# Kernel optimization log

Measured on AMD Instinct MI355X. Metric: run time of the kernel, lower is better.

The kernel has to match this reference:

```python
import jax, jax.numpy as jnp
import numpy as np

B, T, D = 4, 2048, 1024
H = 16
HD = D // H  # 64

def setup_inputs() -> dict:
    key = jax.random.key(0)
    k1, k2, k3 = jax.random.split(key, 3)
    x = jax.random.normal(k1, (B, T, D), dtype=jnp.float32)
    # torch nn.Linear weight layout: [out_features, in_features]
    w_qkv = jax.random.normal(k2, (3 * D, D), dtype=jnp.float32) * (D ** -0.5)
    w_proj = jax.random.normal(k3, (D, D), dtype=jnp.float32) * (D ** -0.5)
    return {"x": x, "w_qkv": w_qkv, "w_proj": w_proj}

def reference(x, w_qkv, w_proj):
    b, t, c = x.shape
    qkv = jnp.einsum('btc,oc->bto', x, w_qkv)  # [b,t,3c]
    q, k, v = jnp.split(qkv, 3, axis=-1)
    # [b,h,t,hd]
    q = q.reshape(b, t, H, HD).transpose(0, 2, 1, 3)
    k = k.reshape(b, t, H, HD).transpose(0, 2, 1, 3)
    v = v.reshape(b, t, H, HD).transpose(0, 2, 1, 3)
    att = jnp.einsum('bhqd,bhkd->bhqk', q, k) / (HD ** 0.5)
    causal = jnp.tril(jnp.ones((t, t), dtype=bool))
    att = jnp.where(causal, att, -jnp.inf)
    att = jax.nn.softmax(att, axis=-1)
    y = jnp.einsum('bhqk,bhkd->bhqd', att, v)
    y = y.transpose(0, 2, 1, 3).reshape(b, t, c)
    return jnp.einsum('btc,oc->bto', y, w_proj)
```

## Files before the change

kernel.cpp:

```cpp
#include <hip/hip_runtime.h>
#include <cstdint>
#include <cstddef>


typedef __bf16 bf16;
typedef __bf16 bf16x4 __attribute__((ext_vector_type(4)));
typedef __bf16 bf16x8 __attribute__((ext_vector_type(8)));
typedef float  f32x4  __attribute__((ext_vector_type(4)));
typedef float  fvec4  __attribute__((ext_vector_type(4)));
typedef unsigned u32x2 __attribute__((ext_vector_type(2)));

typedef __attribute__((address_space(1))) const void global_cv;
typedef __attribute__((address_space(3))) void lds_v;

#define MFMA16(a, b, c) __builtin_amdgcn_mfma_f32_16x16x32_bf16((a), (b), (c), 0, 0, 0)

#define QSCALE 0.18033688f

__device__ __forceinline__ void async_ld16(const bf16* g, bf16* l) {
  __builtin_amdgcn_global_load_lds((global_cv*)g, (lds_v*)l, 16, 0, 0);
}

__device__ __forceinline__ int swz_off(int row, int col) {
  int sr = (row & 7) ^ ((row >> 3) & 7);
  return row * 64 + ((((col >> 3) ^ sr) & 7) * 8) + (col & 7);
}

__device__ __forceinline__ unsigned cvt_pk(float lo, float hi) {
  unsigned r;
  asm("v_cvt_pk_bf16_f32 %0, %1, %2" : "=v"(r) : "v"(lo), "v"(hi));
  return r;
}

__device__ __forceinline__ bf16x8 cvt8(const float* p) {
  fvec4 u = *(const fvec4*)p;
  fvec4 v = *(const fvec4*)(p + 4);
  bf16x8 r;
  r[0] = (bf16)u[0]; r[1] = (bf16)u[1]; r[2] = (bf16)u[2]; r[3] = (bf16)u[3];
  r[4] = (bf16)v[0]; r[5] = (bf16)v[1]; r[6] = (bf16)v[2]; r[7] = (bf16)v[3];
  return r;
}

__global__ void cvt_f32_bf16(const float* __restrict__ s, bf16* __restrict__ d,
                             int n8) {
  int i = blockIdx.x * 256 + threadIdx.x;
  if (i < n8) *(bf16x8*)(d + (size_t)i * 8) = cvt8(s + (size_t)i * 8);
}

__device__ __forceinline__ void qkv_scatter(const f32x4 acc[4][4], int m0, int n0,
                                            int wm, int wn, int quad, int l15,
                                            bf16* Qo, bf16* Ko, bf16* Vo) {
  const int which = n0 >> 10;
  if (which == 2) {
#pragma unroll
    for (int i = 0; i < 4; ++i) {
      const int m = m0 + wm + i * 16 + quad * 4;
      const int b = m >> 11;
      const int t = m & 2047;
#pragma unroll
      for (int j = 0; j < 4; ++j) {
        const int n1 = (n0 + wn + j * 16 + l15) & 1023;
        const int h  = n1 >> 6;
        const int d  = n1 & 63;
        bf16x4 v;
#pragma unroll
        for (int r = 0; r < 4; ++r) v[r] = (bf16)acc[i][j][r];
        *(bf16x4*)(Vo + ((size_t)(b * 16 + h) * 64 + d) * 2048 + t) = v;
      }
    }
    return;
  }
  bf16* dst = (which == 0) ? Qo : Ko;
  const float scale = (which == 0) ? QSCALE : 1.0f;
#pragma unroll
  for (int i = 0; i < 4; ++i) {
    const int m = m0 + wm + i * 16 + quad * 4;
#pragma unroll
    for (int j = 0; j < 4; ++j) {
      const int n  = n0 + wn + j * 16 + l15;
      const int n1 = n & 1023;
      const int h  = n1 >> 6;
      const int d  = n1 & 63;
#pragma unroll
      for (int r = 0; r < 4; ++r) {
        const int mm = m + r;
        const int b  = mm >> 11;
        const int t  = mm & 2047;
        dst[(((size_t)(b * 16 + h)) * 2048 + t) * 64 + d] =
            (bf16)(acc[i][j][r] * scale);
      }
    }
  }
}

__global__ __launch_bounds__(256, 2)
void gemm_qkv_a(const bf16* __restrict__ A, const bf16* __restrict__ B,
                bf16* __restrict__ Qo, bf16* __restrict__ Ko,
                bf16* __restrict__ Vo) {
  __shared__ __align__(16) bf16 As[128 * 32];
  __shared__ __align__(16) bf16 Bs[128 * 32];
  const int K = 1024;

  const int tid  = threadIdx.x;
  const int lane = tid & 63;
  const int wave = tid >> 6;
  const int quad = lane >> 4;
  const int l15  = lane & 15;
  const int wm   = (wave >> 1) * 64;
  const int wn   = (wave & 1) * 64;
  const int m0   = blockIdx.y * 128;
  const int n0   = blockIdx.x * 128;

  f32x4 acc[4][4];
#pragma unroll
  for (int i = 0; i < 4; ++i)
#pragma unroll
    for (int j = 0; j < 4; ++j) acc[i][j] = f32x4{0.f, 0.f, 0.f, 0.f};

  const int r0 = tid >> 2;
  const int c0 = (tid & 3) * 8;
  const bf16* ag0 = A + (size_t)(m0 + r0) * K + c0;
  const bf16* ag1 = A + (size_t)(m0 + 64 + r0) * K + c0;
  const bf16* bg0 = B + (size_t)(n0 + r0) * K + c0;
  const bf16* bg1 = B + (size_t)(n0 + 64 + r0) * K + c0;
  const int lo0 = (wave * 64) * 8;
  const int lo1 = (256 + wave * 64) * 8;

  for (int k0 = 0; k0 < K; k0 += 32) {
    __syncthreads();
    async_ld16(ag0 + k0, As + lo0);
    async_ld16(ag1 + k0, As + lo1);
    async_ld16(bg0 + k0, Bs + lo0);
    async_ld16(bg1 + k0, Bs + lo1);
    __syncthreads();

    bf16x8 af[4], bfr[4];
#pragma unroll
    for (int i = 0; i < 4; ++i)
      af[i] = *(const bf16x8*)(As + (wm + i * 16 + l15) * 32 + quad * 8);
#pragma unroll
    for (int j = 0; j < 4; ++j)
      bfr[j] = *(const bf16x8*)(Bs + (wn + j * 16 + l15) * 32 + quad * 8);
#pragma unroll
    for (int i = 0; i < 4; ++i)
#pragma unroll
      for (int j = 0; j < 4; ++j)
        acc[i][j] = MFMA16(af[i], bfr[j], acc[i][j]);
  }
  qkv_scatter(acc, m0, n0, wm, wn, quad, l15, Qo, Ko, Vo);
}

__global__ __launch_bounds__(256, 2)
void gemm_qkv_f(const float* __restrict__ A, const float* __restrict__ B,
                bf16* __restrict__ Qo, bf16* __restrict__ Ko,
                bf16* __restrict__ Vo) {
  __shared__ __align__(16) bf16 As[128 * 32];
  __shared__ __align__(16) bf16 Bs[128 * 32];
  const int K = 1024;

  const int tid  = threadIdx.x;
  const int lane = tid & 63;
  const int wave = tid >> 6;
  const int quad = lane >> 4;
  const int l15  = lane & 15;
  const int wm   = (wave >> 1) * 64;
  const int wn   = (wave & 1) * 64;
  const int m0   = blockIdx.y * 128;
  const int n0   = blockIdx.x * 128;

  f32x4 acc[4][4];
#pragma unroll
  for (int i = 0; i < 4; ++i)
#pragma unroll
    for (int j = 0; j < 4; ++j) acc[i][j] = f32x4{0.f, 0.f, 0.f, 0.f};

  const int r0 = tid >> 2;
  const int c0 = (tid & 3) * 8;
  const size_t aoff0 = (size_t)(m0 + r0) * K + c0;
  const size_t aoff1 = (size_t)(m0 + 64 + r0) * K + c0;
  const size_t boff0 = (size_t)(n0 + r0) * K + c0;
  const size_t boff1 = (size_t)(n0 + 64 + r0) * K + c0;

  for (int k0 = 0; k0 < K; k0 += 32) {
    bf16x8 va0 = cvt8(A + aoff0 + k0);
    bf16x8 va1 = cvt8(A + aoff1 + k0);
    bf16x8 vb0 = cvt8(B + boff0 + k0);
    bf16x8 vb1 = cvt8(B + boff1 + k0);
    __syncthreads();
    *(bf16x8*)(As + tid * 8)        = va0;
    *(bf16x8*)(As + 2048 + tid * 8) = va1;
    *(bf16x8*)(Bs + tid * 8)        = vb0;
    *(bf16x8*)(Bs + 2048 + tid * 8) = vb1;
    __syncthreads();

    bf16x8 af[4], bfr[4];
#pragma unroll
    for (int i = 0; i < 4; ++i)
      af[i] = *(const bf16x8*)(As + (wm + i * 16 + l15) * 32 + quad * 8);
#pragma unroll
    for (int j = 0; j < 4; ++j)
      bfr[j] = *(const bf16x8*)(Bs + (wn + j * 16 + l15) * 32 + quad * 8);
#pragma unroll
    for (int i = 0; i < 4; ++i)
#pragma unroll
      for (int j = 0; j < 4; ++j)
        acc[i][j] = MFMA16(af[i], bfr[j], acc[i][j]);
  }
  qkv_scatter(acc, m0, n0, wm, wn, quad, l15, Qo, Ko, Vo);
}

__global__ __launch_bounds__(256, 4)
void attn(const bf16* __restrict__ Q, const bf16* __restrict__ Kk,
          const bf16* __restrict__ Vt, bf16* __restrict__ Y) {
  __shared__ __align__(16) bf16 Ks[2][64 * 64];
  __shared__ __align__(16) bf16 Vs[2][64 * 64];
  __shared__ __align__(16) bf16 Ps[4 * 16 * 64];

  const int tid  = threadIdx.x;
  const int wave = tid >> 6;
  const int lane = tid & 63;
  const int quad = lane >> 4;
  const int l15  = lane & 15;

  const int lin  = (int)blockIdx.x + ((int)blockIdx.y << 4);
  const int slot = lin >> 3;
  const int bh   = (lin & 7) * 8 + (slot >> 4);
  const int p    = slot & 15;
  const int b    = bh >> 4;
  const int h    = bh & 15;

  const bf16* Qb = Q  + (size_t)bh * (2048 * 64);
  const bf16* Kb = Kk + (size_t)bh * (2048 * 64);
  const bf16* Vb = Vt + (size_t)bh * (2048 * 64);
  char* Pw = (char*)(Ps + wave * (16 * 64));

  const int r0s = wave * 8 + (lane >> 3);
  const int r1s = r0s + 32;
  const int qch = lane & 7;
  const int co0 = (((qch ^ ((r0s & 7) ^ ((r0s >> 3) & 7)))) & 7) * 8;
  const int co1 = (((qch ^ ((r1s & 7) ^ ((r1s >> 3) & 7)))) & 7) * 8;
  const bf16* kg0 = Kb + (size_t)r0s * 64 + co0;
  const bf16* kg1 = Kb + (size_t)r1s * 64 + co1;
  const bf16* vg0 = Vb + (size_t)r0s * 2048 + co0;
  const bf16* vg1 = Vb + (size_t)r1s * 2048 + co1;
  const int ldsw = wave * 512;

  const int psx   = l15 & 7;
  const int prowb = l15 * 128;
  const int pr0   = prowb + ((quad ^ psx) << 4);
  const int pr1   = prowb + (((4 + quad) ^ psx) << 4);

  const float NEG = -1e30f;

#pragma unroll 1
  for (int pass = 0; pass < 2; ++pass) {
    const int qt = pass ? (31 - p) : p;
    const int q0 = qt * 64;

    const bf16* qp = Qb + (size_t)(q0 + wave * 16 + l15) * 64 + quad * 8;
    bf16x8 qa0 = *(const bf16x8*)qp;
    bf16x8 qa1 = *(const bf16x8*)(qp + 32);

    f32x4 l4 = {0.f, 0.f, 0.f, 0.f};
    f32x4 o[4];
#pragma unroll
    for (int j = 0; j < 4; ++j) o[j] = f32x4{0.f, 0.f, 0.f, 0.f};

    async_ld16(kg0, Ks[0] + ldsw);
    async_ld16(kg1, Ks[0] + 2048 + ldsw);
    async_ld16(vg0, Vs[0] + ldsw);
    async_ld16(vg1, Vs[0] + 2048 + ldsw);
    __syncthreads();

#pragma unroll 1
    for (int kt = 0; kt <= qt; ++kt) {
      const int cur = kt & 1;
      const int k0  = kt * 64;

      if (kt < qt) {
        const int kn = k0 + 64;
        async_ld16(kg0 + (size_t)kn * 64, Ks[cur ^ 1] + ldsw);
        async_ld16(kg1 + (size_t)kn * 64, Ks[cur ^ 1] + 2048 + ldsw);
        async_ld16(vg0 + kn, Vs[cur ^ 1] + ldsw);
        async_ld16(vg1 + kn, Vs[cur ^ 1] + 2048 + ldsw);
      }

      f32x4 s[4];
      __builtin_amdgcn_s_setprio(1);
#pragma unroll
      for (int j = 0; j < 4; ++j) {
        const int kvr = j * 16 + l15;
        bf16x8 k0f = *(const bf16x8*)(Ks[cur] + swz_off(kvr, quad * 8));
        bf16x8 k1f = *(const bf16x8*)(Ks[cur] + swz_off(kvr, 32 + quad * 8));
        f32x4 z = {0.f, 0.f, 0.f, 0.f};
        z = MFMA16(k0f, qa0, z);
        z = MFMA16(k1f, qa1, z);
        s[j] = z;
      }
      __builtin_amdgcn_s_setprio(0);

      if (kt == qt) {
        const int qloc = wave * 16 + l15;
#pragma unroll
        for (int j = 0; j < 4; ++j) {
#pragma unroll
          for (int r = 0; r < 4; ++r) {
            if (16 * j + 4 * quad + r > qloc) s[j][r] = NEG;
          }
        }
      }

#pragma unroll
      for (int j = 0; j < 4; ++j) {
#pragma unroll
        for (int r = 0; r < 4; ++r) s[j][r] = exp2f(s[j][r]);
        l4 += s[j];
      }

#pragma unroll
      for (int j = 0; j < 4; ++j) {
        u32x2 pk;
        pk[0] = cvt_pk(s[j][0], s[j][1]);
        pk[1] = cvt_pk(s[j][2], s[j][3]);
        const int C = 2 * j + (quad >> 1);
        *(u32x2*)(Pw + prowb + (((C ^ psx) << 4) | ((quad & 1) << 3))) = pk;
      }

      bf16x8 pf0 = *(const bf16x8*)(Pw + pr0);
      bf16x8 pf1 = *(const bf16x8*)(Pw + pr1);

      __builtin_amdgcn_s_setprio(1);
#pragma unroll
      for (int j = 0; j < 4; ++j) {
        const int d = j * 16 + l15;
        bf16x8 vf0 = *(const bf16x8*)(Vs[cur] + swz_off(d, quad * 8));
        bf16x8 vf1 = *(const bf16x8*)(Vs[cur] + swz_off(d, 32 + quad * 8));
        o[j] = MFMA16(pf0, vf0, o[j]);
        o[j] = MFMA16(pf1, vf1, o[j]);
      }
      __builtin_amdgcn_s_setprio(0);

      __syncthreads();
    }

    float lf = (l4[0] + l4[1]) + (l4[2] + l4[3]);
    lf += __shfl_xor(lf, 16);
    lf += __shfl_xor(lf, 32);
    float inv[4];
#pragma unroll
    for (int r = 0; r < 4; ++r) inv[r] = 1.0f / __shfl(lf, quad * 4 + r);

#pragma unroll
    for (int j = 0; j < 4; ++j) {
      const int dcol = h * 64 + j * 16 + l15;
#pragma unroll
      for (int r = 0; r < 4; ++r) {
        const int trow = q0 + wave * 16 + quad * 4 + r;
        Y[((size_t)b * 2048 + trow) * 1024 + dcol] = (bf16)(o[j][r] * inv[r]);
      }
    }
  }
}

__global__ __launch_bounds__(256, 2)
void gemm_proj_a(const bf16* __restrict__ A, const bf16* __restrict__ B,
                 float* __restrict__ C) {
  __shared__ __align__(16) bf16 As[128 * 32];
  __shared__ __align__(16) bf16 Bs[128 * 32];
  const int K = 1024, N = 1024;

  const int tid  = threadIdx.x;
  const int lane = tid & 63;
  const int wave = tid >> 6;
  const int quad = lane >> 4;
  const int l15  = lane & 15;
  const int wm   = (wave >> 1) * 64;
  const int wn   = (wave & 1) * 64;
  const int m0   = blockIdx.y * 128;
  const int n0   = blockIdx.x * 128;

  f32x4 acc[4][4];
#pragma unroll
  for (int i = 0; i < 4; ++i)
#pragma unroll
    for (int j = 0; j < 4; ++j) acc[i][j] = f32x4{0.f, 0.f, 0.f, 0.f};

  const int r0 = tid >> 2;
  const int c0 = (tid & 3) * 8;
  const bf16* ag0 = A + (size_t)(m0 + r0) * K + c0;
  const bf16* ag1 = A + (size_t)(m0 + 64 + r0) * K + c0;
  const bf16* bg0 = B + (size_t)(n0 + r0) * K + c0;
  const bf16* bg1 = B + (size_t)(n0 + 64 + r0) * K + c0;
  const int lo0 = (wave * 64) * 8;
  const int lo1 = (256 + wave * 64) * 8;

  for (int k0 = 0; k0 < K; k0 += 32) {
    __syncthreads();
    async_ld16(ag0 + k0, As + lo0);
    async_ld16(ag1 + k0, As + lo1);
    async_ld16(bg0 + k0, Bs + lo0);
    async_ld16(bg1 + k0, Bs + lo1);
    __syncthreads();

    bf16x8 af[4], bfr[4];
#pragma unroll
    for (int i = 0; i < 4; ++i)
      af[i] = *(const bf16x8*)(As + (wm + i * 16 + l15) * 32 + quad * 8);
#pragma unroll
    for (int j = 0; j < 4; ++j)
      bfr[j] = *(const bf16x8*)(Bs + (wn + j * 16 + l15) * 32 + quad * 8);
#pragma unroll
    for (int i = 0; i < 4; ++i)
#pragma unroll
      for (int j = 0; j < 4; ++j)
        acc[i][j] = MFMA16(af[i], bfr[j], acc[i][j]);
  }

#pragma unroll
  for (int i = 0; i < 4; ++i) {
    const int m = m0 + wm + i * 16 + quad * 4;
#pragma unroll
    for (int j = 0; j < 4; ++j) {
      const int n = n0 + wn + j * 16 + l15;
#pragma unroll
      for (int r = 0; r < 4; ++r)
        C[(size_t)(m + r) * N + n] = acc[i][j][r];
    }
  }
}

__global__ __launch_bounds__(256, 2)
void gemm_proj_f(const bf16* __restrict__ A, const float* __restrict__ B,
                 float* __restrict__ C) {
  __shared__ __align__(16) bf16 As[128 * 32];
  __shared__ __align__(16) bf16 Bs[128 * 32];
  const int K = 1024, N = 1024;

  const int tid  = threadIdx.x;
  const int lane = tid & 63;
  const int wave = tid >> 6;
  const int quad = lane >> 4;
  const int l15  = lane & 15;
  const int wm   = (wave >> 1) * 64;
  const int wn   = (wave & 1) * 64;
  const int m0   = blockIdx.y * 128;
  const int n0   = blockIdx.x * 128;

  f32x4 acc[4][4];
#pragma unroll
  for (int i = 0; i < 4; ++i)
#pragma unroll
    for (int j = 0; j < 4; ++j) acc[i][j] = f32x4{0.f, 0.f, 0.f, 0.f};

  const int r0 = tid >> 2;
  const int c0 = (tid & 3) * 8;
  const size_t aoff0 = (size_t)(m0 + r0) * K + c0;
  const size_t aoff1 = (size_t)(m0 + 64 + r0) * K + c0;
  const size_t boff0 = (size_t)(n0 + r0) * K + c0;
  const size_t boff1 = (size_t)(n0 + 64 + r0) * K + c0;

  for (int k0 = 0; k0 < K; k0 += 32) {
    bf16x8 va0 = *(const bf16x8*)(A + aoff0 + k0);
    bf16x8 va1 = *(const bf16x8*)(A + aoff1 + k0);
    bf16x8 vb0 = cvt8(B + boff0 + k0);
    bf16x8 vb1 = cvt8(B + boff1 + k0);
    __syncthreads();
    *(bf16x8*)(As + tid * 8)        = va0;
    *(bf16x8*)(As + 2048 + tid * 8) = va1;
    *(bf16x8*)(Bs + tid * 8)        = vb0;
    *(bf16x8*)(Bs + 2048 + tid * 8) = vb1;
    __syncthreads();

    bf16x8 af[4], bfr[4];
#pragma unroll
    for (int i = 0; i < 4; ++i)
      af[i] = *(const bf16x8*)(As + (wm + i * 16 + l15) * 32 + quad * 8);
#pragma unroll
    for (int j = 0; j < 4; ++j)
      bfr[j] = *(const bf16x8*)(Bs + (wn + j * 16 + l15) * 32 + quad * 8);
#pragma unroll
    for (int i = 0; i < 4; ++i)
#pragma unroll
      for (int j = 0; j < 4; ++j)
        acc[i][j] = MFMA16(af[i], bfr[j], acc[i][j]);
  }

#pragma unroll
  for (int i = 0; i < 4; ++i) {
    const int m = m0 + wm + i * 16 + quad * 4;
#pragma unroll
    for (int j = 0; j < 4; ++j) {
      const int n = n0 + wn + j * 16 + l15;
#pragma unroll
      for (int r = 0; r < 4; ++r)
        C[(size_t)(m + r) * N + n] = acc[i][j][r];
    }
  }
}

extern "C" void kernel_launch(void* const* d_in, const int* in_sizes, int n_in,
                              void* d_out, int out_size, void* d_ws, size_t ws_size,
                              hipStream_t stream) {
  const float* x  = nullptr;
  const float* wq = nullptr;
  const float* wp = nullptr;
  for (int i = 0; i < n_in; ++i) {
    if      (in_sizes[i] == 8388608) x  = (const float*)d_in[i];
    else if (in_sizes[i] == 3145728) wq = (const float*)d_in[i];
    else if (in_sizes[i] == 1048576) wp = (const float*)d_in[i];
  }
  if (!x || !wq || !wp) {
    x = (const float*)d_in[0]; wq = (const float*)d_in[1]; wp = (const float*)d_in[2];
  }

  float* out = (float*)d_out;
  const size_t NE = (size_t)4 * 16 * 2048 * 64;
  bf16* kb = (bf16*)d_ws;
  bf16* vb = kb + NE;
  bf16* qb = vb + NE;
  bf16* yb = qb + NE;
  bf16* xb  = yb + NE;
  bf16* wqb = xb + 8388608;
  bf16* wpb = wqb + 3145728;
  const size_t need = (4 * NE + 8388608 + 3145728 + 1048576) * sizeof(bf16);
  const bool ext = ws_size >= need;

  if (ext) {
    cvt_f32_bf16<<<(8388608 / 8 + 255) / 256, 256, 0, stream>>>(x, xb, 8388608 / 8);
    cvt_f32_bf16<<<(3145728 / 8 + 255) / 256, 256, 0, stream>>>(wq, wqb, 3145728 / 8);
    cvt_f32_bf16<<<(1048576 / 8 + 255) / 256, 256, 0, stream>>>(wp, wpb, 1048576 / 8);
    gemm_qkv_a<<<dim3(24, 64), 256, 0, stream>>>(xb, wqb, qb, kb, vb);
  } else {
    gemm_qkv_f<<<dim3(24, 64), 256, 0, stream>>>(x, wq, qb, kb, vb);
  }

  attn<<<dim3(16, 64), 256, 0, stream>>>(qb, kb, vb, yb);

  if (ext) {
    gemm_proj_a<<<dim3(8, 64), 256, 0, stream>>>(yb, wpb, out);
  } else {
    gemm_proj_f<<<dim3(8, 64), 256, 0, stream>>>(yb, wp, out);
  }
}
```

Baseline: 264.5 us.

## Double-buffer GEMM LDS tiles, remap blocks per XCD, fuse conversion kernels

The bf16 QKV and projection GEMMs now use two LDS buffers, so the async global-to-LDS load for the next K-slice is issued before the current slice's MFMAs. This gives one barrier per iteration instead of two. Block indices are remapped so that tiles sharing the same A or B panels land on the same XCD, which is meant to improve L2 reuse. The three f32-to-bf16 conversion launches are merged into one kernel to save launch overhead. Doubling LDS per block may affect occupancy, and the remap also applies to the fallback kernels.

```diff
diff --git a/kernel.cpp b/kernel.cpp
--- a/kernel.cpp
+++ b/kernel.cpp
@@ -41,10 +41,17 @@
   return r;
 }
 
-__global__ void cvt_f32_bf16(const float* __restrict__ s, bf16* __restrict__ d,
-                             int n8) {
+__global__ void cvt_all(const float* __restrict__ x, const float* __restrict__ wq,
+                        const float* __restrict__ wp, bf16* __restrict__ xb,
+                        bf16* __restrict__ wqb, bf16* __restrict__ wpb) {
   int i = blockIdx.x * 256 + threadIdx.x;
-  if (i < n8) *(bf16x8*)(d + (size_t)i * 8) = cvt8(s + (size_t)i * 8);
+  const float* s;
+  bf16* d;
+  int off;
+  if (i < 1048576)      { s = x;  d = xb;  off = i; }
+  else if (i < 1441792) { s = wq; d = wqb; off = i - 1048576; }
+  else                  { s = wp; d = wpb; off = i - 1441792; }
+  *(bf16x8*)(d + (size_t)off * 8) = cvt8(s + (size_t)off * 8);
 }
 
 __device__ __forceinline__ void qkv_scatter(const f32x4 acc[4][4], int m0, int n0,
@@ -97,8 +104,8 @@
 void gemm_qkv_a(const bf16* __restrict__ A, const bf16* __restrict__ B,
                 bf16* __restrict__ Qo, bf16* __restrict__ Ko,
                 bf16* __restrict__ Vo) {
-  __shared__ __align__(16) bf16 As[128 * 32];
-  __shared__ __align__(16) bf16 Bs[128 * 32];
+  __shared__ __align__(16) bf16 As[2][128 * 32];
+  __shared__ __align__(16) bf16 Bs[2][128 * 32];
   const int K = 1024;
 
   const int tid  = threadIdx.x;
@@ -108,8 +115,12 @@
   const int l15  = lane & 15;
   const int wm   = (wave >> 1) * 64;
   const int wn   = (wave & 1) * 64;
-  const int m0   = blockIdx.y * 128;
-  const int n0   = blockIdx.x * 128;
+
+  const int lin = (int)blockIdx.x + (int)blockIdx.y * 24;
+  const int xcd = lin & 7;
+  const int sl  = lin >> 3;
+  const int n0  = (xcd * 3 + (sl % 3)) * 128;
+  const int m0  = (sl / 3) * 128;
 
   f32x4 acc[4][4];
 #pragma unroll
@@ -126,26 +137,36 @@
   const int lo0 = (wave * 64) * 8;
   const int lo1 = (256 + wave * 64) * 8;
 
-  for (int k0 = 0; k0 < K; k0 += 32) {
-    __syncthreads();
-    async_ld16(ag0 + k0, As + lo0);
-    async_ld16(ag1 + k0, As + lo1);
-    async_ld16(bg0 + k0, Bs + lo0);
-    async_ld16(bg1 + k0, Bs + lo1);
-    __syncthreads();
+  async_ld16(ag0, As[0] + lo0);
+  async_ld16(ag1, As[0] + lo1);
+  async_ld16(bg0, Bs[0] + lo0);
+  async_ld16(bg1, Bs[0] + lo1);
+  __syncthreads();
+
+  for (int it = 0; it < 32; ++it) {
+    const int cur = it & 1;
+    if (it < 31) {
+      const int kn = (it + 1) * 32;
+      async_ld16(ag0 + kn, As[cur ^ 1] + lo0);
+      async_ld16(ag1 + kn, As[cur ^ 1] + lo1);
+      async_ld16(bg0 + kn, Bs[cur ^ 1] + lo0);
+      async_ld16(bg1 + kn, Bs[cur ^ 1] + lo1);
+    }
 
     bf16x8 af[4], bfr[4];
 #pragma unroll
     for (int i = 0; i < 4; ++i)
-      af[i] = *(const bf16x8*)(As + (wm + i * 16 + l15) * 32 + quad * 8);
+      af[i] = *(const bf16x8*)(As[cur] + (wm + i * 16 + l15) * 32 + quad * 8);
 #pragma unroll
     for (int j = 0; j < 4; ++j)
-      bfr[j] = *(const bf16x8*)(Bs + (wn + j * 16 + l15) * 32 + quad * 8);
+      bfr[j] = *(const bf16x8*)(Bs[cur] + (wn + j * 16 + l15) * 32 + quad * 8);
 #pragma unroll
     for (int i = 0; i < 4; ++i)
 #pragma unroll
       for (int j = 0; j < 4; ++j)
         acc[i][j] = MFMA16(af[i], bfr[j], acc[i][j]);
+
+    __syncthreads();
   }
   qkv_scatter(acc, m0, n0, wm, wn, quad, l15, Qo, Ko, Vo);
 }
@@ -165,8 +186,12 @@
   const int l15  = lane & 15;
   const int wm   = (wave >> 1) * 64;
   const int wn   = (wave & 1) * 64;
-  const int m0   = blockIdx.y * 128;
-  const int n0   = blockIdx.x * 128;
+
+  const int lin = (int)blockIdx.x + (int)blockIdx.y * 24;
+  const int xcd = lin & 7;
+  const int sl  = lin >> 3;
+  const int n0  = (xcd * 3 + (sl % 3)) * 128;
+  const int m0  = (sl / 3) * 128;
 
   f32x4 acc[4][4];
 #pragma unroll
@@ -365,8 +390,8 @@
 __global__ __launch_bounds__(256, 2)
 void gemm_proj_a(const bf16* __restrict__ A, const bf16* __restrict__ B,
                  float* __restrict__ C) {
-  __shared__ __align__(16) bf16 As[128 * 32];
-  __shared__ __align__(16) bf16 Bs[128 * 32];
+  __shared__ __align__(16) bf16 As[2][128 * 32];
+  __shared__ __align__(16) bf16 Bs[2][128 * 32];
   const int K = 1024, N = 1024;
 
   const int tid  = threadIdx.x;
@@ -376,8 +401,12 @@
   const int l15  = lane & 15;
   const int wm   = (wave >> 1) * 64;
   const int wn   = (wave & 1) * 64;
-  const int m0   = blockIdx.y * 128;
-  const int n0   = blockIdx.x * 128;
+
+  const int lin = (int)blockIdx.x + (int)blockIdx.y * 8;
+  const int xcd = lin & 7;
+  const int sl  = lin >> 3;
+  const int m0  = (xcd * 8 + (sl & 7)) * 128;
+  const int n0  = (sl >> 3) * 128;
 
   f32x4 acc[4][4];
 #pragma unroll
@@ -394,26 +423,36 @@
   const int lo0 = (wave * 64) * 8;
   const int lo1 = (256 + wave * 64) * 8;
 
-  for (int k0 = 0; k0 < K; k0 += 32) {
-    __syncthreads();
-    async_ld16(ag0 + k0, As + lo0);
-    async_ld16(ag1 + k0, As + lo1);
-    async_ld16(bg0 + k0, Bs + lo0);
-    async_ld16(bg1 + k0, Bs + lo1);
-    __syncthreads();
+  async_ld16(ag0, As[0] + lo0);
+  async_ld16(ag1, As[0] + lo1);
+  async_ld16(bg0, Bs[0] + lo0);
+  async_ld16(bg1, Bs[0] + lo1);
+  __syncthreads();
+
+  for (int it = 0; it < 32; ++it) {
+    const int cur = it & 1;
+    if (it < 31) {
+      const int kn = (it + 1) * 32;
+      async_ld16(ag0 + kn, As[cur ^ 1] + lo0);
+      async_ld16(ag1 + kn, As[cur ^ 1] + lo1);
+      async_ld16(bg0 + kn, Bs[cur ^ 1] + lo0);
+      async_ld16(bg1 + kn, Bs[cur ^ 1] + lo1);
+    }
 
     bf16x8 af[4], bfr[4];
 #pragma unroll
     for (int i = 0; i < 4; ++i)
-      af[i] = *(const bf16x8*)(As + (wm + i * 16 + l15) * 32 + quad * 8);
+      af[i] = *(const bf16x8*)(As[cur] + (wm + i * 16 + l15) * 32 + quad * 8);
 #pragma unroll
     for (int j = 0; j < 4; ++j)
-      bfr[j] = *(const bf16x8*)(Bs + (wn + j * 16 + l15) * 32 + quad * 8);
+      bfr[j] = *(const bf16x8*)(Bs[cur] + (wn + j * 16 + l15) * 32 + quad * 8);
 #pragma unroll
     for (int i = 0; i < 4; ++i)
 #pragma unroll
       for (int j = 0; j < 4; ++j)
         acc[i][j] = MFMA16(af[i], bfr[j], acc[i][j]);
+
+    __syncthreads();
   }
 
 #pragma unroll
@@ -443,8 +482,12 @@
   const int l15  = lane & 15;
   const int wm   = (wave >> 1) * 64;
   const int wn   = (wave & 1) * 64;
-  const int m0   = blockIdx.y * 128;
-  const int n0   = blockIdx.x * 128;
+
+  const int lin = (int)blockIdx.x + (int)blockIdx.y * 8;
+  const int xcd = lin & 7;
+  const int sl  = lin >> 3;
+  const int m0  = (xcd * 8 + (sl & 7)) * 128;
+  const int n0  = (sl >> 3) * 128;
 
   f32x4 acc[4][4];
 #pragma unroll
@@ -526,9 +569,7 @@
   const bool ext = ws_size >= need;
 
   if (ext) {
-    cvt_f32_bf16<<<(8388608 / 8 + 255) / 256, 256, 0, stream>>>(x, xb, 8388608 / 8);
-    cvt_f32_bf16<<<(3145728 / 8 + 255) / 256, 256, 0, stream>>>(wq, wqb, 3145728 / 8);
-    cvt_f32_bf16<<<(1048576 / 8 + 255) / 256, 256, 0, stream>>>(wp, wpb, 1048576 / 8);
+    cvt_all<<<6144, 256, 0, stream>>>(x, wq, wp, xb, wqb, wpb);
     gemm_qkv_a<<<dim3(24, 64), 256, 0, stream>>>(xb, wqb, qb, kb, vb);
   } else {
     gemm_qkv_f<<<dim3(24, 64), 256, 0, stream>>>(x, wq, qb, kb, vb);
```

After: 257.0 us. 2.8% less time.
